# Optimization experiments

Hardware: AMD Instinct MI355X
Metric: run time of the kernel (lower is better)

The kernel has to match this reference:

```python
import jax, jax.numpy as jnp
import numpy as np

NSAMPLE = 32
LAMBDA = 0.5


def setup_inputs() -> dict:
    key = jax.random.key(0)
    k1, k2, k3, k4, k5 = jax.random.split(key, 5)
    B, N, NPOINT, C, NCOMP = 4, 8192, 2048, 64, 16
    xyz = jax.random.normal(k1, (B, N, 3), dtype=jnp.float32)
    new_xyz = jax.random.normal(k2, (B, NPOINT, 3), dtype=jnp.float32)
    components = jax.random.randint(k3, (B, N, 1), 0, NCOMP, dtype=jnp.int64)
    new_components = jax.random.randint(k4, (B, NPOINT, 1), 0, NCOMP, dtype=jnp.int64)
    features = jax.random.normal(k5, (B, C, N), dtype=jnp.float32)
    return {"xyz": xyz, "new_xyz": new_xyz, "components": components,
            "new_components": new_components, "features": features}


def _gag_knn(new_xyz, xyz, new_comp, comp, k, lam):
    # squared pairwise distances (B, npoint, N), same math as sum((src-dst)**2)
    diff = new_xyz[:, :, None, :] - xyz[:, None, :, :]
    dists = jnp.sum(diff * diff, axis=-1)
    # component-aware rescale
    mask = comp[:, None, :] == new_comp[:, :, None]  # (B, npoint, N)
    dists = jnp.where(mask, dists * lam, dists * (1.0 - lam))
    # full argsort then take first k (faithful to original)
    idx = jnp.argsort(dists, axis=-1)[:, :, :k]  # (B, npoint, k)
    return idx.astype(jnp.int32)


def reference(xyz, new_xyz, components, new_components, features):
    comp = components[..., 0]
    new_comp = new_components[..., 0]
    idx = _gag_knn(new_xyz, xyz, new_comp, comp, NSAMPLE, LAMBDA)  # (B, npoint, ns)

    # group xyz: gather along N -> (B, npoint, ns, 3)
    grouped_xyz = jnp.take_along_axis(xyz[:, None, :, :], idx[..., None], axis=2)
    grouped_xyz = grouped_xyz - new_xyz[:, :, None, :]
    grouped_xyz = jnp.transpose(grouped_xyz, (0, 3, 1, 2))  # (B, 3, npoint, ns)

    # group features: (B, C, N) -> (B, npoint, ns, C) -> (B, C, npoint, ns)
    feats_bnc = jnp.transpose(features, (0, 2, 1))  # (B, N, C)
    grouped_feats = jnp.take_along_axis(feats_bnc[:, None, :, :], idx[..., None], axis=2)
    grouped_feats = jnp.transpose(grouped_feats, (0, 3, 1, 2))  # (B, C, npoint, ns)

    return jnp.concatenate([grouped_xyz, grouped_feats], axis=1)  # (B, 3+C, npoint, ns)
```

## Files before the change

### kernel.cpp

```cpp
#include <hip/hip_runtime.h>


#define BQ 4
#define NN_ 8192
#define NPOINT 2048
#define CF 64
#define NS 32
#define T1 256
#define PER (NN_ / T1)
#define QB 4
#define CAPQ 192
#define M_EPS 1e-3f

#define KNN_BLOCKS (BQ * NPOINT / QB)
#define TR_BLOCKS  ((NN_ / 32) * (CF / 32) * BQ)

__global__ __launch_bounds__(256) void knn_tr_kernel(
    const float* __restrict__ xyz, const float* __restrict__ new_xyz,
    const float* __restrict__ features, int* __restrict__ idxOut,
    float* __restrict__ featsT) {
  const int tid = threadIdx.x;

  if (blockIdx.x >= KNN_BLOCKS) {
    const int t = blockIdx.x - KNN_BLOCKS;
    const int n0 = (t & 255) * 32;
    const int c0 = ((t >> 8) & 1) * 32;
    const int b = t >> 9;
    const int tx = tid & 31;
    const int ty = tid >> 5;
    __shared__ float tr[32][33];
#pragma unroll
    for (int i = 0; i < 4; i++) {
      int c = c0 + ty + i * 8;
      tr[ty + i * 8][tx] = features[(size_t)b * CF * NN_ + (size_t)c * NN_ + n0 + tx];
    }
    __syncthreads();
#pragma unroll
    for (int i = 0; i < 4; i++) {
      int nrow = n0 + ty + i * 8;
      featsT[(size_t)b * NN_ * CF + (size_t)nrow * CF + c0 + tx] = tr[tx][ty + i * 8];
    }
    return;
  }

  const int tile = blockIdx.x;
  const int b = tile / (NPOINT / QB);
  const int q0 = b * NPOINT + (tile % (NPOINT / QB)) * QB;
  const int lane = tid & 63;
  const int wid = tid >> 6;

  float qx[QB], qy[QB], qz[QB], qn[QB];
#pragma unroll
  for (int k = 0; k < QB; k++) {
    qx[k] = new_xyz[(q0 + k) * 3 + 0];
    qy[k] = new_xyz[(q0 + k) * 3 + 1];
    qz[k] = new_xyz[(q0 + k) * 3 + 2];
    qn[k] = qx[k] * qx[k] + qy[k] * qy[k] + qz[k] * qz[k];
  }

  const float4* __restrict__ base4 =
      (const float4*)(xyz + (size_t)b * NN_ * 3);

  float smin_r[QB];
#pragma unroll
  for (int k = 0; k < QB; k++) smin_r[k] = 3.4e38f;

#pragma unroll
  for (int g = 0; g < PER / 4; g++) {
    const int v = g * 768 + tid * 3;
    float4 v0 = base4[v + 0];
    float4 v1 = base4[v + 1];
    float4 v2 = base4[v + 2];
    float xs[4] = {v0.x, v0.w, v1.z, v2.y};
    float ys[4] = {v0.y, v1.x, v1.w, v2.z};
    float zs[4] = {v0.z, v1.y, v2.x, v2.w};
#pragma unroll
    for (int i = 0; i < 4; i++) {
      float pp = xs[i] * xs[i] + ys[i] * ys[i] + zs[i] * zs[i];
#pragma unroll
      for (int k = 0; k < QB; k++) {
        float dot = xs[i] * qx[k] + ys[i] * qy[k] + zs[i] * qz[k];
        smin_r[k] = fminf(smin_r[k], pp - 2.0f * dot);
      }
    }
  }

  __shared__ float sMin[QB][T1];
  __shared__ float sTheta[QB];
  __shared__ unsigned long long cand[QB][CAPQ];
  __shared__ int cnt[QB];
#pragma unroll
  for (int k = 0; k < QB; k++) sMin[k][tid] = smin_r[k];
  if (tid < QB) cnt[tid] = 0;
  __syncthreads();

  {
    const int k = wid;
    float m = fminf(fminf(sMin[k][lane], sMin[k][lane + 64]),
                    fminf(sMin[k][lane + 128], sMin[k][lane + 192]));
#pragma unroll
    for (int kk = 2; kk <= 64; kk <<= 1) {
#pragma unroll
      for (int jj = kk >> 1; jj > 0; jj >>= 1) {
        float o = __shfl_xor(m, jj);
        bool up = ((lane & kk) == 0);
        bool lower = ((lane & jj) == 0);
        m = (up == lower) ? fminf(m, o) : fmaxf(m, o);
      }
    }
    if (lane == 31) sTheta[k] = m + qn[k] + M_EPS;
  }
  __syncthreads();

  float thd[QB];
#pragma unroll
  for (int k = 0; k < QB; k++) thd[k] = sTheta[k];

#pragma unroll
  for (int g = 0; g < PER / 4; g++) {
    const int v = g * 768 + tid * 3;
    float4 v0 = base4[v + 0];
    float4 v1 = base4[v + 1];
    float4 v2 = base4[v + 2];
    float xs[4] = {v0.x, v0.w, v1.z, v2.y};
    float ys[4] = {v0.y, v1.x, v1.w, v2.z};
    float zs[4] = {v0.z, v1.y, v2.x, v2.w};
#pragma unroll
    for (int i = 0; i < 4; i++) {
      float pp = xs[i] * xs[i] + ys[i] * ys[i] + zs[i] * zs[i];
#pragma unroll
      for (int k = 0; k < QB; k++) {
        float dot = xs[i] * qx[k] + ys[i] * qy[k] + zs[i] * qz[k];
        float s = pp - 2.0f * dot + qn[k];
        if (s <= thd[k] + M_EPS) {
          float dx = xs[i] - qx[k], dy = ys[i] - qy[k], dz = zs[i] - qz[k];
          float d = __fadd_rn(__fadd_rn(__fmul_rn(dx, dx), __fmul_rn(dy, dy)),
                              __fmul_rn(dz, dz));
          if (d <= thd[k]) {
            int n = g * 1024 + tid * 4 + i;
            int pos = atomicAdd(&cnt[k], 1);
            if (pos < CAPQ)
              cand[k][pos] =
                  ((unsigned long long)__float_as_uint(d) << 32) | (unsigned)n;
          }
        }
      }
    }
  }
  __syncthreads();

  {
    const int k = wid;
    const int m = cnt[k] < CAPQ ? cnt[k] : CAPQ;
    for (int i = lane; i < m; i += 64) {
      unsigned long long x = cand[k][i];
      int r = 0;
      for (int j = 0; j < m; j++) r += (cand[k][j] < x) ? 1 : 0;
      if (r < NS) idxOut[(q0 + k) * NS + r] = (int)(x & 0xffffffffu);
    }
  }
}

#define FSTR 68
__global__ __launch_bounds__(256) void group_kernel(const float* __restrict__ xyz,
                                                    const float* __restrict__ new_xyz,
                                                    const float* __restrict__ featsT,
                                                    const int* __restrict__ idxArr,
                                                    float* __restrict__ out) {
  const int q = blockIdx.x;
  const int b = q / NPOINT;
  const int p = q - b * NPOINT;
  const int tid = threadIdx.x;

  __shared__ int sIdx[NS];
  __shared__ __align__(16) float ldsF[NS * FSTR];
  __shared__ float ldsX[3 * NS];

  if (tid < NS) sIdx[tid] = idxArr[q * NS + tid];
  __syncthreads();

  {
    int s = tid >> 3, r = tid & 7;
    int nn = sIdx[s];
    const float4* src = (const float4*)(featsT + ((size_t)b * NN_ + nn) * CF);
    float4 v0 = src[r * 2];
    float4 v1 = src[r * 2 + 1];
    float4* dst = (float4*)(ldsF + s * FSTR + r * 8);
    dst[0] = v0;
    dst[1] = v1;
  }
  if (tid < 96) {
    int dd = tid >> 5, s = tid & 31;
    int nn = sIdx[s];
    ldsX[dd * NS + s] = xyz[((size_t)b * NN_ + nn) * 3 + dd] -
                        new_xyz[(size_t)q * 3 + dd];
  }
  __syncthreads();

  const int s = tid & 31;
  const int r0 = tid >> 5;
#pragma unroll
  for (int k = 0; k < 9; k++) {
    int row = r0 + k * 8;
    if (row < 67) {
      float v = (row < 3) ? ldsX[row * NS + s] : ldsF[s * FSTR + (row - 3)];
      out[(((size_t)b * 67 + row) * NPOINT + p) * NS + s] = v;
    }
  }
}

extern "C" void kernel_launch(void* const* d_in, const int* in_sizes, int n_in,
                              void* d_out, int out_size, void* d_ws, size_t ws_size,
                              hipStream_t stream) {
  const float* xyz      = (const float*)d_in[0];
  const float* new_xyz  = (const float*)d_in[1];
  const float* features = (const float*)d_in[4];
  float* out = (float*)d_out;

  int* idxArr = (int*)d_ws;
  float* featsT = (float*)((char*)d_ws + (size_t)BQ * NPOINT * NS * sizeof(int));

  knn_tr_kernel<<<KNN_BLOCKS + TR_BLOCKS, T1, 0, stream>>>(xyz, new_xyz, features,
                                                           idxArr, featsT);
  group_kernel<<<BQ * NPOINT, T1, 0, stream>>>(xyz, new_xyz, featsT, idxArr, out);
}
```

Measured before the change: 134.9 us.

## Process eight queries per KNN block with FMA distance and scalarized query constants

Doubles the number of query points handled per KNN block so each loaded xyz point is reused across more queries, halving the number of passes over the point cloud. Distance computations are rewritten as FMA chains with premultiplied -2q coefficients, and query constants and thresholds are forced into scalar registers via readfirstlane. Shared memory is unioned between the transpose and KNN paths to hold the larger per-block buffers. The trade-off is higher register pressure and fewer KNN blocks, which may reduce occupancy and parallelism.

```diff
diff --git a/kernel.cpp b/kernel.cpp
--- a/kernel.cpp
+++ b/kernel.cpp
@@ -8,27 +8,34 @@
 #define NS 32
 #define T1 256
 #define PER (NN_ / T1)
-#define QB 4
+#define QB 8
 #define CAPQ 192
 #define M_EPS 1e-3f
 
 #define KNN_BLOCKS (BQ * NPOINT / QB)
 #define TR_BLOCKS  ((NN_ / 32) * (CF / 32) * BQ)
+
+#define SMEM_BYTES (QB * T1 * 4 + QB * CAPQ * 8 + QB * 4 + QB * 4)
+
+__device__ __forceinline__ float rfl(float x) {
+  return __int_as_float(__builtin_amdgcn_readfirstlane(__float_as_int(x)));
+}
 
 __global__ __launch_bounds__(256) void knn_tr_kernel(
     const float* __restrict__ xyz, const float* __restrict__ new_xyz,
     const float* __restrict__ features, int* __restrict__ idxOut,
     float* __restrict__ featsT) {
+  __shared__ __align__(16) char smem[SMEM_BYTES];
   const int tid = threadIdx.x;
 
   if (blockIdx.x >= KNN_BLOCKS) {
+    float(*tr)[33] = (float(*)[33])smem;
     const int t = blockIdx.x - KNN_BLOCKS;
     const int n0 = (t & 255) * 32;
     const int c0 = ((t >> 8) & 1) * 32;
     const int b = t >> 9;
     const int tx = tid & 31;
     const int ty = tid >> 5;
-    __shared__ float tr[32][33];
 #pragma unroll
     for (int i = 0; i < 4; i++) {
       int c = c0 + ty + i * 8;
@@ -42,6 +49,12 @@
     }
     return;
   }
+
+  float(*sMin)[T1] = (float(*)[T1])smem;
+  unsigned long long(*cand)[CAPQ] =
+      (unsigned long long(*)[CAPQ])(smem + QB * T1 * 4);
+  float* sTheta = (float*)(smem + QB * T1 * 4 + QB * CAPQ * 8);
+  int* cnt = (int*)(smem + QB * T1 * 4 + QB * CAPQ * 8 + QB * 4);
 
   const int tile = blockIdx.x;
   const int b = tile / (NPOINT / QB);
@@ -49,17 +62,19 @@
   const int lane = tid & 63;
   const int wid = tid >> 6;
 
-  float qx[QB], qy[QB], qz[QB], qn[QB];
+  float qx2[QB], qy2[QB], qz2[QB], qnn[QB];
 #pragma unroll
   for (int k = 0; k < QB; k++) {
-    qx[k] = new_xyz[(q0 + k) * 3 + 0];
-    qy[k] = new_xyz[(q0 + k) * 3 + 1];
-    qz[k] = new_xyz[(q0 + k) * 3 + 2];
-    qn[k] = qx[k] * qx[k] + qy[k] * qy[k] + qz[k] * qz[k];
-  }
-
-  const float4* __restrict__ base4 =
-      (const float4*)(xyz + (size_t)b * NN_ * 3);
+    float ax = new_xyz[(q0 + k) * 3 + 0];
+    float ay = new_xyz[(q0 + k) * 3 + 1];
+    float az = new_xyz[(q0 + k) * 3 + 2];
+    qx2[k] = rfl(-2.0f * ax);
+    qy2[k] = rfl(-2.0f * ay);
+    qz2[k] = rfl(-2.0f * az);
+    qnn[k] = rfl(ax * ax + ay * ay + az * az);
+  }
+
+  const float4* __restrict__ base4 = (const float4*)(xyz + (size_t)b * NN_ * 3);
 
   float smin_r[QB];
 #pragma unroll
@@ -76,26 +91,25 @@
     float zs[4] = {v0.z, v1.y, v2.x, v2.w};
 #pragma unroll
     for (int i = 0; i < 4; i++) {
-      float pp = xs[i] * xs[i] + ys[i] * ys[i] + zs[i] * zs[i];
+      float pp = fmaf(zs[i], zs[i], fmaf(ys[i], ys[i], xs[i] * xs[i]));
 #pragma unroll
       for (int k = 0; k < QB; k++) {
-        float dot = xs[i] * qx[k] + ys[i] * qy[k] + zs[i] * qz[k];
-        smin_r[k] = fminf(smin_r[k], pp - 2.0f * dot);
+        float t = fmaf(xs[i], qx2[k], pp);
+        t = fmaf(ys[i], qy2[k], t);
+        t = fmaf(zs[i], qz2[k], t);
+        smin_r[k] = fminf(smin_r[k], t);
       }
     }
   }
 
-  __shared__ float sMin[QB][T1];
-  __shared__ float sTheta[QB];
-  __shared__ unsigned long long cand[QB][CAPQ];
-  __shared__ int cnt[QB];
 #pragma unroll
   for (int k = 0; k < QB; k++) sMin[k][tid] = smin_r[k];
   if (tid < QB) cnt[tid] = 0;
   __syncthreads();
 
-  {
-    const int k = wid;
+#pragma unroll
+  for (int t2 = 0; t2 < 2; t2++) {
+    const int k = wid * 2 + t2;
     float m = fminf(fminf(sMin[k][lane], sMin[k][lane + 64]),
                     fminf(sMin[k][lane + 128], sMin[k][lane + 192]));
 #pragma unroll
@@ -108,13 +122,16 @@
         m = (up == lower) ? fminf(m, o) : fmaxf(m, o);
       }
     }
-    if (lane == 31) sTheta[k] = m + qn[k] + M_EPS;
-  }
-  __syncthreads();
-
-  float thd[QB];
-#pragma unroll
-  for (int k = 0; k < QB; k++) thd[k] = sTheta[k];
+    if (lane == 31) sTheta[k] = m + qnn[k] + M_EPS;
+  }
+  __syncthreads();
+
+  float thd[QB], th2[QB];
+#pragma unroll
+  for (int k = 0; k < QB; k++) {
+    thd[k] = rfl(sTheta[k]);
+    th2[k] = rfl(thd[k] + M_EPS - qnn[k]);
+  }
 
 #pragma unroll
   for (int g = 0; g < PER / 4; g++) {
@@ -127,13 +144,16 @@
     float zs[4] = {v0.z, v1.y, v2.x, v2.w};
 #pragma unroll
     for (int i = 0; i < 4; i++) {
-      float pp = xs[i] * xs[i] + ys[i] * ys[i] + zs[i] * zs[i];
+      float pp = fmaf(zs[i], zs[i], fmaf(ys[i], ys[i], xs[i] * xs[i]));
 #pragma unroll
       for (int k = 0; k < QB; k++) {
-        float dot = xs[i] * qx[k] + ys[i] * qy[k] + zs[i] * qz[k];
-        float s = pp - 2.0f * dot + qn[k];
-        if (s <= thd[k] + M_EPS) {
-          float dx = xs[i] - qx[k], dy = ys[i] - qy[k], dz = zs[i] - qz[k];
+        float t = fmaf(xs[i], qx2[k], pp);
+        t = fmaf(ys[i], qy2[k], t);
+        t = fmaf(zs[i], qz2[k], t);
+        if (t <= th2[k]) {
+          float dx = xs[i] - (-0.5f * qx2[k]);
+          float dy = ys[i] - (-0.5f * qy2[k]);
+          float dz = zs[i] - (-0.5f * qz2[k]);
           float d = __fadd_rn(__fadd_rn(__fmul_rn(dx, dx), __fmul_rn(dy, dy)),
                               __fmul_rn(dz, dz));
           if (d <= thd[k]) {
@@ -149,8 +169,9 @@
   }
   __syncthreads();
 
-  {
-    const int k = wid;
+#pragma unroll
+  for (int t2 = 0; t2 < 2; t2++) {
+    const int k = wid * 2 + t2;
     const int m = cnt[k] < CAPQ ? cnt[k] : CAPQ;
     for (int i = lane; i < m; i += 64) {
       unsigned long long x = cand[k][i];
```

After: 134.0 us. About the same (-0.6%).
